# Kernel tuning notes

Hardware: AMD Instinct MI355X
Metric: run time of the kernel (lower is better)

## Reference

```python
import jax, jax.numpy as jnp
import numpy as np

N = 100000   # nodes
E = 1600000  # edges (avg degree 16)
D = 64       # in_dim == emb_dim
L = 3        # num_layers
G = 2000     # graphs in batch
LN_EPS = 1e-5


def setup_inputs() -> dict:
    key = jax.random.key(0)
    ks = jax.random.split(key, 14)
    s = 0.05  # xavier-ish small init scale
    x = jax.random.normal(ks[0], (N, D), jnp.float32)
    edge_index = jax.random.randint(ks[1], (2, E), 0, N, dtype=jnp.int32)
    batch = jnp.sort(jax.random.randint(ks[2], (N,), 0, G, dtype=jnp.int32))
    return {
        "x": x,
        "edge_index": edge_index,
        "batch": batch,
        # stacked per-layer GIN MLP params: Linear(D,D) -> SiLU -> Linear(D,D)
        "W1": jax.random.normal(ks[3], (L, D, D), jnp.float32) * s,
        "b1": jnp.zeros((L, D), jnp.float32),
        "W2": jax.random.normal(ks[4], (L, D, D), jnp.float32) * s,
        "b2": jnp.zeros((L, D), jnp.float32),
        "eps": jnp.zeros((L,), jnp.float32),  # trainable eps, init 0
        "ln_g": jnp.ones((L, D), jnp.float32),
        "ln_b": jnp.zeros((L, D), jnp.float32),
        # gate_nn: Linear(D, D//2) -> SiLU -> Linear(D//2, 1)
        "gw1": jax.random.normal(ks[5], (D, D // 2), jnp.float32) * s,
        "gb1": jnp.zeros((D // 2,), jnp.float32),
        "gw2": jax.random.normal(ks[6], (D // 2, 1), jnp.float32) * s,
        "gb2": jnp.zeros((1,), jnp.float32),
    }


def _layernorm(h, g, b):
    mu = jnp.mean(h, axis=-1, keepdims=True)
    var = jnp.mean(jnp.square(h - mu), axis=-1, keepdims=True)
    return (h - mu) * jax.lax.rsqrt(var + LN_EPS) * g + b


def reference(x, edge_index, batch, W1, b1, W2, b2, eps, ln_g, ln_b, gw1, gb1, gw2, gb2):
    src, dst = edge_index[0], edge_index[1]
    # ---- GIN layers (eval mode: dropout is identity) ----
    for l in range(L):
        agg = jax.ops.segment_sum(x[src], dst, num_segments=N)  # scatter-add of neighbor feats
        h = (1.0 + eps[l]) * x + agg                             # GIN update
        h = jax.nn.silu(h @ W1[l] + b1[l]) @ W2[l] + b2[l]       # 2-layer MLP
        x = _layernorm(h, ln_g[l], ln_b[l])
    # ---- GlobalAttention pooling ----
    gate = (jax.nn.silu(x @ gw1 + gb1) @ gw2 + gb2)[:, 0]        # [N]
    m = jax.ops.segment_max(gate, batch, num_segments=G)         # per-graph max for stability
    e = jnp.exp(gate - m[batch])
    denom = jax.ops.segment_sum(e, batch, num_segments=G)
    a = e / denom[batch]                                         # per-graph softmax
    out = jax.ops.segment_sum(a[:, None] * x, batch, num_segments=G)  # [G, D]
    return out
```

## Files before the change

kernel.cpp:

```cpp
#include <hip/hip_runtime.h>
#include <math.h>

#define NN 100000
#define NE 1600000
#define D 64
#define NG 2000
#define LN_EPS 1e-5f
#define NB ((NN + 255) / 256)
#define NBK NB
#define NTILE ((NN + 63) / 64)
#define EPB 6400
#define NPART (NE / EPB)
#define CAP 6144
#define LSTR 72
#define WFRAG_MLP 24576
#define WFRAG_TOT 26624
#define CONV1K ((NN * D) / 1024)
#define WPREP1K (WFRAG_TOT / 1024)

typedef __attribute__((ext_vector_type(8))) short short8;
typedef __attribute__((ext_vector_type(8))) unsigned short ushort8;
typedef __attribute__((ext_vector_type(4))) float floatx4;

__device__ __forceinline__ unsigned short f2bf(float f) {
    unsigned int u = __float_as_uint(f);
    u += 0x7FFF + ((u >> 16) & 1);
    return (unsigned short)(u >> 16);
}
__device__ __forceinline__ float bfu2f(unsigned short v) {
    return __uint_as_float(((unsigned int)v) << 16);
}

__global__ __launch_bounds__(1024) void k_prep_part(const float* __restrict__ x,
                                                    unsigned short* __restrict__ xb,
                                                    const float* __restrict__ W1,
                                                    const float* __restrict__ W2,
                                                    const float* __restrict__ gw1,
                                                    unsigned short* __restrict__ wfrag,
                                                    const int* __restrict__ src,
                                                    const int* __restrict__ dst,
                                                    int* __restrict__ bcur,
                                                    unsigned int* __restrict__ colbuf) {
    __shared__ int lcnt[NBK];
    __shared__ int lbase[NBK];
    int b = blockIdx.x;
    int tid = threadIdx.x;

    if (b < NPART) {
        int e0 = b * EPB;
        for (int i = tid; i < NBK; i += 1024) lcnt[i] = 0;
        __syncthreads();

        for (int e = tid; e < EPB; e += 1024)
            atomicAdd(&lcnt[dst[e0 + e] >> 8], 1);
        __syncthreads();

        for (int i = tid; i < NBK; i += 1024) {
            int c = lcnt[i];
            lbase[i] = c ? (i * CAP + atomicAdd(&bcur[i * 16], c)) : 0;
            lcnt[i] = 0;
        }
        __syncthreads();

        for (int e = tid; e < EPB; e += 1024) {
            int d = dst[e0 + e];
            int s = src[e0 + e];
            int bk = d >> 8;
            int pos = lbase[bk] + atomicAdd(&lcnt[bk], 1);
            colbuf[pos] = ((unsigned int)s << 8) | (unsigned int)(d & 255);
        }
    } else if (b < NPART + CONV1K) {
        int i = (b - NPART) * 1024 + tid;
        xb[i] = f2bf(x[i]);
    } else {
        int idx = (b - NPART - CONV1K) * 1024 + tid;
        if (idx < WFRAG_MLP) {
            int l = idx / 8192;
            int rem = idx % 8192;
            int mat = rem / 4096;
            int r2 = rem % 4096;
            int ks = r2 / 2048;
            int c = (r2 / 512) % 4;
            int lane = (r2 / 8) % 64;
            int j = r2 % 8;
            int n = lane & 15, q = lane >> 4;
            int k = ks * 32 + q * 8 + j;
            int col = c * 16 + n;
            const float* Wm = mat ? W2 : W1;
            wfrag[idx] = f2bf(Wm[l * 4096 + k * 64 + col]);
        } else {
            int g = idx - WFRAG_MLP;
            int ks = g / 1024;
            int c = (g / 512) % 2;
            int lane = (g / 8) % 64;
            int j = g % 8;
            int n = lane & 15, q = lane >> 4;
            int k = ks * 32 + q * 8 + j;
            wfrag[idx] = f2bf(gw1[k * 32 + c * 16 + n]);
        }
    }
}

__global__ __launch_bounds__(256) void k_bfill(const unsigned int* __restrict__ colbuf,
                                               const int* __restrict__ bcur,
                                               int* __restrict__ rps,
                                               int* __restrict__ rpe,
                                               int* __restrict__ col) {
    __shared__ int lcur[256];
    __shared__ int wsum[4];
    int b = blockIdx.x;
    int ebase = b * CAP;
    int cnt = bcur[b * 16];
    int nb0 = b * 256;
    int nodes = min(256, NN - nb0);
    int tid = threadIdx.x;
    int lane = tid & 63;
    int w = tid >> 6;

    lcur[tid] = 0;
    __syncthreads();

    for (int e = tid; e < cnt; e += 256)
        atomicAdd(&lcur[colbuf[ebase + e] & 255], 1);
    __syncthreads();

    int v = lcur[tid];
    int x = v;
#pragma unroll
    for (int off = 1; off < 64; off <<= 1) {
        int u = __shfl_up(x, off, 64);
        if (lane >= off) x += u;
    }
    if (lane == 63) wsum[w] = x;
    __syncthreads();
    int base = ebase;
    for (int k = 0; k < w; k++) base += wsum[k];
    int rp = base + x - v;
    if (tid < nodes) {
        rps[nb0 + tid] = rp;
        rpe[nb0 + tid] = rp + v;
    }
    lcur[tid] = rp;
    __syncthreads();

    for (int e = tid; e < cnt; e += 256) {
        unsigned int p = colbuf[ebase + e];
        int pos = atomicAdd(&lcur[p & 255], 1);
        col[pos] = p >> 8;
    }
}

__global__ __launch_bounds__(256) void k_gather(const unsigned short* __restrict__ xin,
                                                unsigned short* __restrict__ h,
                                                const int* __restrict__ rps,
                                                const int* __restrict__ rpe,
                                                const int* __restrict__ col,
                                                const float* __restrict__ epsp) {
    int w = threadIdx.x >> 6;
    int lane = threadIdx.x & 63;
    int g = lane >> 3;
    int fl = lane & 7;
    int node = (blockIdx.x * 4 + w) * 8 + g;
    int start = rps[node], end = rpe[node];

    ushort8 xs = *(const ushort8*)(xin + ((size_t)node << 6) + fl * 8);

    float a0 = 0.f, a1 = 0.f, a2 = 0.f, a3 = 0.f, a4 = 0.f, a5 = 0.f, a6 = 0.f, a7 = 0.f;
    int eb = start;
    for (; eb + 8 <= end; eb += 8) {
        int c = col[eb + fl];
        ushort8 v[8];
#pragma unroll
        for (int j = 0; j < 8; j++) {
            int idx = __shfl(c, g * 8 + j, 64);
            v[j] = *(const ushort8*)(xin + ((size_t)idx << 6) + fl * 8);
        }
#pragma unroll
        for (int j = 0; j < 8; j++) {
            a0 += bfu2f(v[j][0]); a1 += bfu2f(v[j][1]);
            a2 += bfu2f(v[j][2]); a3 += bfu2f(v[j][3]);
            a4 += bfu2f(v[j][4]); a5 += bfu2f(v[j][5]);
            a6 += bfu2f(v[j][6]); a7 += bfu2f(v[j][7]);
        }
    }
    if (eb < end) {
        int cnt = end - eb;
        int c = (fl < cnt) ? col[eb + fl] : 0;
        int j = 0;
        for (; j + 4 <= cnt; j += 4) {
            int i0 = __shfl(c, g * 8 + j, 64);
            int i1 = __shfl(c, g * 8 + j + 1, 64);
            int i2 = __shfl(c, g * 8 + j + 2, 64);
            int i3 = __shfl(c, g * 8 + j + 3, 64);
            ushort8 v0 = *(const ushort8*)(xin + ((size_t)i0 << 6) + fl * 8);
            ushort8 v1 = *(const ushort8*)(xin + ((size_t)i1 << 6) + fl * 8);
            ushort8 v2 = *(const ushort8*)(xin + ((size_t)i2 << 6) + fl * 8);
            ushort8 v3 = *(const ushort8*)(xin + ((size_t)i3 << 6) + fl * 8);
            a0 += bfu2f(v0[0]) + bfu2f(v1[0]) + bfu2f(v2[0]) + bfu2f(v3[0]);
            a1 += bfu2f(v0[1]) + bfu2f(v1[1]) + bfu2f(v2[1]) + bfu2f(v3[1]);
            a2 += bfu2f(v0[2]) + bfu2f(v1[2]) + bfu2f(v2[2]) + bfu2f(v3[2]);
            a3 += bfu2f(v0[3]) + bfu2f(v1[3]) + bfu2f(v2[3]) + bfu2f(v3[3]);
            a4 += bfu2f(v0[4]) + bfu2f(v1[4]) + bfu2f(v2[4]) + bfu2f(v3[4]);
            a5 += bfu2f(v0[5]) + bfu2f(v1[5]) + bfu2f(v2[5]) + bfu2f(v3[5]);
            a6 += bfu2f(v0[6]) + bfu2f(v1[6]) + bfu2f(v2[6]) + bfu2f(v3[6]);
            a7 += bfu2f(v0[7]) + bfu2f(v1[7]) + bfu2f(v2[7]) + bfu2f(v3[7]);
        }
        for (; j < cnt; j++) {
            int i0 = __shfl(c, g * 8 + j, 64);
            ushort8 v0 = *(const ushort8*)(xin + ((size_t)i0 << 6) + fl * 8);
            a0 += bfu2f(v0[0]); a1 += bfu2f(v0[1]);
            a2 += bfu2f(v0[2]); a3 += bfu2f(v0[3]);
            a4 += bfu2f(v0[4]); a5 += bfu2f(v0[5]);
            a6 += bfu2f(v0[6]); a7 += bfu2f(v0[7]);
        }
    }
    float ev = 1.0f + *epsp;
    ushort8 o;
    o[0] = f2bf(ev * bfu2f(xs[0]) + a0);
    o[1] = f2bf(ev * bfu2f(xs[1]) + a1);
    o[2] = f2bf(ev * bfu2f(xs[2]) + a2);
    o[3] = f2bf(ev * bfu2f(xs[3]) + a3);
    o[4] = f2bf(ev * bfu2f(xs[4]) + a4);
    o[5] = f2bf(ev * bfu2f(xs[5]) + a5);
    o[6] = f2bf(ev * bfu2f(xs[6]) + a6);
    o[7] = f2bf(ev * bfu2f(xs[7]) + a7);
    *(ushort8*)(h + ((size_t)node << 6) + fl * 8) = o;
}

template <int LAST>
__global__ __launch_bounds__(256) void k_mfma(const unsigned short* __restrict__ h,
                                              unsigned short* __restrict__ xout,
                                              const short8* __restrict__ wf,
                                              const short8* __restrict__ gf,
                                              const float* __restrict__ b1,
                                              const float* __restrict__ b2,
                                              const float* __restrict__ lng,
                                              const float* __restrict__ lnb,
                                              const float* __restrict__ gb1,
                                              const float* __restrict__ gw2,
                                              const float* __restrict__ gb2,
                                              float* __restrict__ gate) {
    __shared__ __align__(16) unsigned short a2[4][16 * LSTR];
    int w = threadIdx.x >> 6;
    int lane = threadIdx.x & 63;
    int n = lane & 15;
    int q = lane >> 4;
    int base = blockIdx.x * 64 + w * 16;

    short8 B1f[2][4], B2f[2][4];
#pragma unroll
    for (int ks = 0; ks < 2; ks++)
#pragma unroll
        for (int c = 0; c < 4; c++) {
            B1f[ks][c] = wf[(ks * 4 + c) * 64 + lane];
            B2f[ks][c] = wf[512 + (ks * 4 + c) * 64 + lane];
        }
    short8 B3f[2][2];
    if (LAST) {
#pragma unroll
        for (int ks = 0; ks < 2; ks++)
#pragma unroll
            for (int c = 0; c < 2; c++)
                B3f[ks][c] = gf[(ks * 2 + c) * 64 + lane];
    }

    float b1v[4], b2v[4], lgv[4], lbv[4];
#pragma unroll
    for (int c = 0; c < 4; c++) {
        b1v[c] = b1[c * 16 + n];
        b2v[c] = b2[c * 16 + n];
        lgv[c] = lng[c * 16 + n];
        lbv[c] = lnb[c * 16 + n];
    }
    float gb1v[2], gw2v[2], gb2v = 0.f;
    if (LAST) {
        gb1v[0] = gb1[n]; gb1v[1] = gb1[16 + n];
        gw2v[0] = gw2[n]; gw2v[1] = gw2[16 + n];
        gb2v = gb2[0];
    }

    unsigned short* aw = a2[w];

    int mnode = base + n;
    int mc = min(mnode, NN - 1);
    const short8* hp = (const short8*)(h + ((size_t)mc << 6));
    short8 A0 = hp[q];
    short8 A1 = hp[4 + q];

    floatx4 acc1[4];
#pragma unroll
    for (int c = 0; c < 4; c++) {
        floatx4 a = {b1v[c], b1v[c], b1v[c], b1v[c]};
        a = __builtin_amdgcn_mfma_f32_16x16x32_bf16(A0, B1f[0][c], a, 0, 0, 0);
        a = __builtin_amdgcn_mfma_f32_16x16x32_bf16(A1, B1f[1][c], a, 0, 0, 0);
        acc1[c] = a;
    }

#pragma unroll
    for (int c = 0; c < 4; c++)
#pragma unroll
        for (int r = 0; r < 4; r++) {
            float v = acc1[c][r];
            v = v / (1.0f + __expf(-v));
            aw[(q * 4 + r) * LSTR + c * 16 + n] = f2bf(v);
        }

    const short8* ap = (const short8*)(aw + n * LSTR);
    short8 A20 = ap[q];
    short8 A21 = ap[4 + q];

    floatx4 acc2[4];
#pragma unroll
    for (int c = 0; c < 4; c++) {
        floatx4 a = {b2v[c], b2v[c], b2v[c], b2v[c]};
        a = __builtin_amdgcn_mfma_f32_16x16x32_bf16(A20, B2f[0][c], a, 0, 0, 0);
        a = __builtin_amdgcn_mfma_f32_16x16x32_bf16(A21, B2f[1][c], a, 0, 0, 0);
        acc2[c] = a;
    }

    float mu[4], inv[4];
#pragma unroll
    for (int r = 0; r < 4; r++) {
        float s = acc2[0][r] + acc2[1][r] + acc2[2][r] + acc2[3][r];
#pragma unroll
        for (int off = 1; off < 16; off <<= 1) s += __shfl_xor(s, off, 64);
        mu[r] = s * (1.0f / 64.0f);
        float d0 = acc2[0][r] - mu[r], d1 = acc2[1][r] - mu[r];
        float d2 = acc2[2][r] - mu[r], d3 = acc2[3][r] - mu[r];
        float vv = d0 * d0 + d1 * d1 + d2 * d2 + d3 * d3;
#pragma unroll
        for (int off = 1; off < 16; off <<= 1) vv += __shfl_xor(vv, off, 64);
        inv[r] = rsqrtf(vv * (1.0f / 64.0f) + LN_EPS);
    }

#pragma unroll
    for (int c = 0; c < 4; c++)
#pragma unroll
        for (int r = 0; r < 4; r++) {
            int node = base + q * 4 + r;
            float o = (acc2[c][r] - mu[r]) * inv[r] * lgv[c] + lbv[c];
            unsigned short ob = f2bf(o);
            if (node < NN) xout[((size_t)node << 6) + c * 16 + n] = ob;
            if (LAST) aw[(q * 4 + r) * LSTR + c * 16 + n] = ob;
        }

    if (LAST) {
        short8 G0 = ap[q];
        short8 G1 = ap[4 + q];
        floatx4 acc3[2];
#pragma unroll
        for (int c = 0; c < 2; c++) {
            floatx4 a = {gb1v[c], gb1v[c], gb1v[c], gb1v[c]};
            a = __builtin_amdgcn_mfma_f32_16x16x32_bf16(G0, B3f[0][c], a, 0, 0, 0);
            a = __builtin_amdgcn_mfma_f32_16x16x32_bf16(G1, B3f[1][c], a, 0, 0, 0);
            acc3[c] = a;
        }
#pragma unroll
        for (int r = 0; r < 4; r++) {
            float v0 = acc3[0][r];
            v0 = v0 / (1.0f + __expf(-v0));
            float v1 = acc3[1][r];
            v1 = v1 / (1.0f + __expf(-v1));
            float gsum = v0 * gw2v[0] + v1 * gw2v[1];
#pragma unroll
            for (int off = 1; off < 16; off <<= 1) gsum += __shfl_xor(gsum, off, 64);
            int node = base + q * 4 + r;
            if (n == 0 && node < NN) gate[node] = gsum + gb2v;
        }
    }
}

__global__ __launch_bounds__(256) void k_pool(const unsigned short* __restrict__ xf,
                                              const float* __restrict__ gate,
                                              const int* __restrict__ batch,
                                              float* __restrict__ out) {
    __shared__ float redm[4];
    __shared__ float reds[4];
    __shared__ float racc[4][D];
    int g = blockIdx.x;
    int w = threadIdx.x >> 6;
    int lane = threadIdx.x & 63;

    int lo = 0, hi = NN;
    while (lo < hi) { int mid = (lo + hi) >> 1; if (batch[mid] < g) lo = mid + 1; else hi = mid; }
    int start = lo;
    hi = NN;
    while (lo < hi) { int mid = (lo + hi) >> 1; if (batch[mid] < g + 1) lo = mid + 1; else hi = mid; }
    int end = lo;

    if (start >= end) {
        if (w == 0) out[((size_t)g << 6) + lane] = 0.0f;
        return;
    }

    float m = -INFINITY;
    for (int i = start + (int)threadIdx.x; i < end; i += 256) m = fmaxf(m, gate[i]);
#pragma unroll
    for (int mm = 32; mm >= 1; mm >>= 1) m = fmaxf(m, __shfl_xor(m, mm, 64));
    if (lane == 0) redm[w] = m;
    __syncthreads();
    m = fmaxf(fmaxf(redm[0], redm[1]), fmaxf(redm[2], redm[3]));

    float s = 0.0f;
    for (int i = start + (int)threadIdx.x; i < end; i += 256) s += __expf(gate[i] - m);
#pragma unroll
    for (int mm = 32; mm >= 1; mm >>= 1) s += __shfl_xor(s, mm, 64);
    if (lane == 0) reds[w] = s;
    __syncthreads();
    s = (reds[0] + reds[1]) + (reds[2] + reds[3]);

    float acc = 0.0f;
    for (int i = start + w; i < end; i += 4)
        acc += __expf(gate[i] - m) * bfu2f(xf[((size_t)i << 6) + lane]);
    racc[w][lane] = acc;
    __syncthreads();
    if (w == 0)
        out[((size_t)g << 6) + lane] =
            ((racc[0][lane] + racc[1][lane]) + (racc[2][lane] + racc[3][lane])) / s;
}

extern "C" void kernel_launch(void* const* d_in, const int* in_sizes, int n_in,
                              void* d_out, int out_size, void* d_ws, size_t ws_size,
                              hipStream_t stream) {
    const float* x   = (const float*)d_in[0];
    const int* ei    = (const int*)d_in[1];
    const int* batch = (const int*)d_in[2];
    const float* W1  = (const float*)d_in[3];
    const float* b1  = (const float*)d_in[4];
    const float* W2  = (const float*)d_in[5];
    const float* b2  = (const float*)d_in[6];
    const float* eps = (const float*)d_in[7];
    const float* lng = (const float*)d_in[8];
    const float* lnb = (const float*)d_in[9];
    const float* gw1 = (const float*)d_in[10];
    const float* gb1 = (const float*)d_in[11];
    const float* gw2 = (const float*)d_in[12];
    const float* gb2 = (const float*)d_in[13];

    const int* src = ei;
    const int* dst = ei + NE;

    unsigned short* xb    = (unsigned short*)d_ws;
    unsigned short* h     = xb + (size_t)NN * D;
    float* gate           = (float*)(h + (size_t)NN * D);
    int* rps              = (int*)(gate + NN);
    int* rpe              = rps + NN;
    int* colbuf           = rpe + NN;
    int* col              = colbuf + (size_t)NBK * CAP;
    int* bcur             = col + (size_t)NBK * CAP;
    unsigned short* wfrag = (unsigned short*)(bcur + NBK * 16);

    float* out = (float*)d_out;

    hipMemsetAsync(bcur, 0, NBK * 16 * sizeof(int), stream);
    k_prep_part<<<NPART + CONV1K + WPREP1K, 1024, 0, stream>>>(
        x, xb, W1, W2, gw1, wfrag, src, dst, bcur, (unsigned int*)colbuf);
    k_bfill<<<NBK, 256, 0, stream>>>((unsigned int*)colbuf, bcur, rps, rpe, col);

    const short8* wf0 = (const short8*)(wfrag);
    const short8* wf1 = (const short8*)(wfrag + 8192);
    const short8* wf2 = (const short8*)(wfrag + 16384);
    const short8* gf  = (const short8*)(wfrag + WFRAG_MLP);

    k_gather<<<NN / 32, 256, 0, stream>>>(xb, h, rps, rpe, col, eps + 0);
    k_mfma<0><<<NTILE, 256, 0, stream>>>(h, xb, wf0, gf,
        b1 + 0 * D, b2 + 0 * D, lng + 0 * D, lnb + 0 * D, gb1, gw2, gb2, gate);

    k_gather<<<NN / 32, 256, 0, stream>>>(xb, h, rps, rpe, col, eps + 1);
    k_mfma<0><<<NTILE, 256, 0, stream>>>(h, xb, wf1, gf,
        b1 + 1 * D, b2 + 1 * D, lng + 1 * D, lnb + 1 * D, gb1, gw2, gb2, gate);

    k_gather<<<NN / 32, 256, 0, stream>>>(xb, h, rps, rpe, col, eps + 2);
    k_mfma<1><<<NTILE, 256, 0, stream>>>(h, xb, wf2, gf,
        b1 + 2 * D, b2 + 2 * D, lng + 2 * D, lnb + 2 * D, gb1, gw2, gb2, gate);

    k_pool<<<NG, 256, 0, stream>>>(xb, gate, batch, out);
}
```

Before: 292.6 us.

## Fuse neighbor gather and MLP/LayerNorm into one per-layer kernel

Merges the gather kernel and the MFMA MLP+LayerNorm kernel into a single 512-thread kernel per layer. Each 64-node tile is aggregated by 8 waves into shared memory, then 4 waves run the MLP on that tile. Inputs and outputs ping-pong between two buffers. This removes the global write and re-read of the intermediate h buffer and three kernel launches. In exchange, half the waves sit idle during the MLP phase, and the larger block with more LDS may lower occupancy for the latency-bound gather.

```diff
diff --git a/kernel.cpp b/kernel.cpp
--- a/kernel.cpp
+++ b/kernel.cpp
@@ -150,20 +150,36 @@
     }
 }
 
-__global__ __launch_bounds__(256) void k_gather(const unsigned short* __restrict__ xin,
-                                                unsigned short* __restrict__ h,
-                                                const int* __restrict__ rps,
-                                                const int* __restrict__ rpe,
-                                                const int* __restrict__ col,
-                                                const float* __restrict__ epsp) {
+template <int LAST>
+__global__ __launch_bounds__(512) void k_layer(const unsigned short* __restrict__ xin,
+                                               unsigned short* __restrict__ xout,
+                                               const int* __restrict__ rps,
+                                               const int* __restrict__ rpe,
+                                               const int* __restrict__ col,
+                                               const float* __restrict__ epsp,
+                                               const short8* __restrict__ wf,
+                                               const short8* __restrict__ gf,
+                                               const float* __restrict__ b1,
+                                               const float* __restrict__ b2,
+                                               const float* __restrict__ lng,
+                                               const float* __restrict__ lnb,
+                                               const float* __restrict__ gb1,
+                                               const float* __restrict__ gw2,
+                                               const float* __restrict__ gb2,
+                                               float* __restrict__ gate) {
+    __shared__ __align__(16) unsigned short smH[64 * LSTR];
+    __shared__ __align__(16) unsigned short smA[4][16 * LSTR];
     int w = threadIdx.x >> 6;
     int lane = threadIdx.x & 63;
     int g = lane >> 3;
     int fl = lane & 7;
-    int node = (blockIdx.x * 4 + w) * 8 + g;
-    int start = rps[node], end = rpe[node];
-
-    ushort8 xs = *(const ushort8*)(xin + ((size_t)node << 6) + fl * 8);
+    int bl = w * 8 + g;
+    int node = blockIdx.x * 64 + bl;
+    int nc = min(node, NN - 1);
+    int start = rps[nc];
+    int end = (node < NN) ? rpe[nc] : start;
+
+    ushort8 xs = *(const ushort8*)(xin + ((size_t)nc << 6) + fl * 8);
 
     float a0 = 0.f, a1 = 0.f, a2 = 0.f, a3 = 0.f, a4 = 0.f, a5 = 0.f, a6 = 0.f, a7 = 0.f;
     int eb = start;
@@ -214,35 +230,22 @@
             a6 += bfu2f(v0[6]); a7 += bfu2f(v0[7]);
         }
     }
-    float ev = 1.0f + *epsp;
-    ushort8 o;
-    o[0] = f2bf(ev * bfu2f(xs[0]) + a0);
-    o[1] = f2bf(ev * bfu2f(xs[1]) + a1);
-    o[2] = f2bf(ev * bfu2f(xs[2]) + a2);
-    o[3] = f2bf(ev * bfu2f(xs[3]) + a3);
-    o[4] = f2bf(ev * bfu2f(xs[4]) + a4);
-    o[5] = f2bf(ev * bfu2f(xs[5]) + a5);
-    o[6] = f2bf(ev * bfu2f(xs[6]) + a6);
-    o[7] = f2bf(ev * bfu2f(xs[7]) + a7);
-    *(ushort8*)(h + ((size_t)node << 6) + fl * 8) = o;
-}
-
-template <int LAST>
-__global__ __launch_bounds__(256) void k_mfma(const unsigned short* __restrict__ h,
-                                              unsigned short* __restrict__ xout,
-                                              const short8* __restrict__ wf,
-                                              const short8* __restrict__ gf,
-                                              const float* __restrict__ b1,
-                                              const float* __restrict__ b2,
-                                              const float* __restrict__ lng,
-                                              const float* __restrict__ lnb,
-                                              const float* __restrict__ gb1,
-                                              const float* __restrict__ gw2,
-                                              const float* __restrict__ gb2,
-                                              float* __restrict__ gate) {
-    __shared__ __align__(16) unsigned short a2[4][16 * LSTR];
-    int w = threadIdx.x >> 6;
-    int lane = threadIdx.x & 63;
+    {
+        float ev = 1.0f + *epsp;
+        ushort8 o;
+        o[0] = f2bf(ev * bfu2f(xs[0]) + a0);
+        o[1] = f2bf(ev * bfu2f(xs[1]) + a1);
+        o[2] = f2bf(ev * bfu2f(xs[2]) + a2);
+        o[3] = f2bf(ev * bfu2f(xs[3]) + a3);
+        o[4] = f2bf(ev * bfu2f(xs[4]) + a4);
+        o[5] = f2bf(ev * bfu2f(xs[5]) + a5);
+        o[6] = f2bf(ev * bfu2f(xs[6]) + a6);
+        o[7] = f2bf(ev * bfu2f(xs[7]) + a7);
+        *(ushort8*)(smH + bl * LSTR + fl * 8) = o;
+    }
+    __syncthreads();
+
+    if (w >= 4) return;
     int n = lane & 15;
     int q = lane >> 4;
     int base = blockIdx.x * 64 + w * 16;
@@ -279,11 +282,9 @@
         gb2v = gb2[0];
     }
 
-    unsigned short* aw = a2[w];
-
-    int mnode = base + n;
-    int mc = min(mnode, NN - 1);
-    const short8* hp = (const short8*)(h + ((size_t)mc << 6));
+    unsigned short* aw = smA[w];
+
+    const short8* hp = (const short8*)(smH + (w * 16 + n) * LSTR);
     short8 A0 = hp[q];
     short8 A1 = hp[4 + q];
 
@@ -337,10 +338,10 @@
     for (int c = 0; c < 4; c++)
 #pragma unroll
         for (int r = 0; r < 4; r++) {
-            int node = base + q * 4 + r;
+            int onode = base + q * 4 + r;
             float o = (acc2[c][r] - mu[r]) * inv[r] * lgv[c] + lbv[c];
             unsigned short ob = f2bf(o);
-            if (node < NN) xout[((size_t)node << 6) + c * 16 + n] = ob;
+            if (onode < NN) xout[((size_t)onode << 6) + c * 16 + n] = ob;
             if (LAST) aw[(q * 4 + r) * LSTR + c * 16 + n] = ob;
         }
 
@@ -364,8 +365,8 @@
             float gsum = v0 * gw2v[0] + v1 * gw2v[1];
 #pragma unroll
             for (int off = 1; off < 16; off <<= 1) gsum += __shfl_xor(gsum, off, 64);
-            int node = base + q * 4 + r;
-            if (n == 0 && node < NN) gate[node] = gsum + gb2v;
+            int onode = base + q * 4 + r;
+            if (n == 0 && onode < NN) gate[onode] = gsum + gb2v;
         }
     }
 }
@@ -462,17 +463,14 @@
     const short8* wf2 = (const short8*)(wfrag + 16384);
     const short8* gf  = (const short8*)(wfrag + WFRAG_MLP);
 
-    k_gather<<<NN / 32, 256, 0, stream>>>(xb, h, rps, rpe, col, eps + 0);
-    k_mfma<0><<<NTILE, 256, 0, stream>>>(h, xb, wf0, gf,
+    k_layer<0><<<NTILE, 512, 0, stream>>>(xb, h, rps, rpe, col, eps + 0, wf0, gf,
         b1 + 0 * D, b2 + 0 * D, lng + 0 * D, lnb + 0 * D, gb1, gw2, gb2, gate);
 
-    k_gather<<<NN / 32, 256, 0, stream>>>(xb, h, rps, rpe, col, eps + 1);
-    k_mfma<0><<<NTILE, 256, 0, stream>>>(h, xb, wf1, gf,
+    k_layer<0><<<NTILE, 512, 0, stream>>>(h, xb, rps, rpe, col, eps + 1, wf1, gf,
         b1 + 1 * D, b2 + 1 * D, lng + 1 * D, lnb + 1 * D, gb1, gw2, gb2, gate);
 
-    k_gather<<<NN / 32, 256, 0, stream>>>(xb, h, rps, rpe, col, eps + 2);
-    k_mfma<1><<<NTILE, 256, 0, stream>>>(h, xb, wf2, gf,
+    k_layer<1><<<NTILE, 512, 0, stream>>>(xb, h, rps, rpe, col, eps + 2, wf2, gf,
         b1 + 2 * D, b2 + 2 * D, lng + 2 * D, lnb + 2 * D, gb1, gw2, gb2, gate);
 
-    k_pool<<<NG, 256, 0, stream>>>(xb, gate, batch, out);
-}
+    k_pool<<<NG, 256, 0, stream>>>(h, gate, batch, out);
+}
```

Result: faster. 286.6 us (-2.1%).
